# Optimization experiments

Measured on AMD Instinct MI355X. Metric: run time of the kernel, lower is better.

## Reference

```python
import jax, jax.numpy as jnp
import numpy as np

NUM_DIRECTIONS = 32
RESOLUTION = 64
SCALE = 8.0
RADIUS_MULT = 1.1
SEED = 17


def _directions(num_directions, seed):
    # mirrors _generate_uniform_directions: randn columns normalized to unit norm
    v = jax.random.normal(jax.random.key(seed), (3, num_directions), dtype=jnp.float32)
    v = v / jnp.clip(jnp.sqrt(jnp.sum(v * v, axis=0, keepdims=True)), 1e-12)
    return v  # [3, D]


def _grid(spatial_shape):
    # voxel coordinates on [-1,1]^3 lattice, flattened to [P, 3]
    axes = [jnp.linspace(-1.0, 1.0, s, dtype=jnp.float32) for s in spatial_shape]
    coords = jnp.stack(jnp.meshgrid(*axes, indexing='ij'), axis=-1).reshape(-1, 3)
    radius = RADIUS_MULT * jnp.max(jnp.sqrt(jnp.sum(coords * coords, axis=-1)))
    return coords, radius


def _ect(weights, coords, dirs, radius):
    # weights: [B, P, C]; coords: [P, 3]; dirs: [3, D]
    nh = coords @ dirs                                   # [P, D] projections
    lin = jnp.linspace(-radius, radius, RESOLUTION)      # [R] thresholds
    # soft indicator: sigmoid(scale * (t - <x, v>))  -> [R, P, D]
    ecc = jax.nn.sigmoid(SCALE * (lin[:, None, None] - nh[None, :, :]))
    # accumulate per (batch, class, threshold, direction)
    return jnp.einsum('bpc,rpd->bcrd', weights, ecc)     # [B, C, R, D]


def _forward(prediction, target):
    B, C = prediction.shape[0], prediction.shape[1]
    spatial = prediction.shape[2:]
    coords, radius = _grid(spatial)
    dirs = _directions(NUM_DIRECTIONS, SEED)
    # apply_activation='auto' with C>1 -> softmax over channel dim
    act = jax.nn.softmax(prediction.astype(jnp.float32), axis=1)
    w_pred = act.reshape(B, C, -1).transpose(0, 2, 1)    # [B, P, C]
    # target: class indices -> one-hot float (prepared target, no activation)
    tgt_oh = jax.nn.one_hot(target, C, axis=1, dtype=jnp.float32)  # [B, C, X, Y, Z]
    w_tgt = tgt_oh.reshape(B, C, -1).transpose(0, 2, 1)  # [B, P, C]
    ect_pred = _ect(w_pred, coords, dirs, radius)
    ect_tgt = _ect(w_tgt, coords, dirs, radius)
    # aggregation='mse'
    return jnp.mean((ect_pred - ect_tgt) ** 2)


def setup_inputs() -> dict:
    key = jax.random.key(0)
    k1, k2 = jax.random.split(key)
    prediction = jax.random.normal(k1, (2, 3, 48, 48, 48), dtype=jnp.float32)
    target = jax.random.randint(k2, (2, 48, 48, 48), 0, 3, dtype=jnp.int64)
    return {"prediction": prediction, "target": target}


def reference(prediction, target):
    return _forward(prediction, target)
```

## Files before the change

### kernel.cpp

```cpp
#include <hip/hip_runtime.h>
#include <cstdint>


#define P_TOT 110592
#define VOX 216
#define GRID 512
#define NREP 4

__device__ __forceinline__ uint32_t rotl32(uint32_t x, int d) {
  return (x << d) | (x >> (32 - d));
}

__device__ __forceinline__ void threefry_0_17(uint32_t x0, uint32_t x1,
                                              uint32_t& o0, uint32_t& o1) {
  const uint32_t ks0 = 0u, ks1 = 17u, ks2 = 0x1BD11BDAu ^ 0u ^ 17u;
  x0 += ks0; x1 += ks1;
#define R4(a,b,c,dd) \
  x0 += x1; x1 = rotl32(x1,(a)); x1 ^= x0; \
  x0 += x1; x1 = rotl32(x1,(b)); x1 ^= x0; \
  x0 += x1; x1 = rotl32(x1,(c)); x1 ^= x0; \
  x0 += x1; x1 = rotl32(x1,(dd)); x1 ^= x0;
  R4(13,15,26,6)   x0 += ks1; x1 += ks2 + 1u;
  R4(17,29,16,24)  x0 += ks2; x1 += ks0 + 2u;
  R4(13,15,26,6)   x0 += ks0; x1 += ks1 + 3u;
  R4(17,29,16,24)  x0 += ks1; x1 += ks2 + 4u;
  R4(13,15,26,6)   x0 += ks2; x1 += ks0 + 5u;
#undef R4
  o0 = x0; o1 = x1;
}

__device__ __forceinline__ float erfinv_f32(float x) {
  float w = -log1pf(-x * x);
  float p;
  if (w < 5.0f) {
    w = w - 2.5f;
    p = 2.81022636e-08f;
    p = fmaf(p, w, 3.43273939e-07f);
    p = fmaf(p, w, -3.5233877e-06f);
    p = fmaf(p, w, -4.39150654e-06f);
    p = fmaf(p, w, 0.00021858087f);
    p = fmaf(p, w, -0.00125372503f);
    p = fmaf(p, w, -0.00417768164f);
    p = fmaf(p, w, 0.246640727f);
    p = fmaf(p, w, 1.50140941f);
  } else {
    w = sqrtf(w) - 3.0f;
    p = -0.000200214257f;
    p = fmaf(p, w, 0.000100950558f);
    p = fmaf(p, w, 0.00134934322f);
    p = fmaf(p, w, 0.000337081863f);
    p = fmaf(p, w, 0.00573950773f);
    p = fmaf(p, w, -0.0076224613f);
    p = fmaf(p, w, 0.00943887047f);
    p = fmaf(p, w, 1.00167406f);
    p = fmaf(p, w, 2.83297682f);
  }
  return p * x;
}

__device__ __forceinline__ void ect_block_compute(
    const float* __restrict__ pred, const int* __restrict__ tgt,
    float* dirs, float4* voxdw, float4* voxc,
    int t, int bx, float acc[8][4]) {
  const int d = t & 31;
  const int rg = t >> 5;
  const int cbase = bx * VOX;

  if (t < 96) {
    uint32_t o0, o1;
    threefry_0_17(0u, (uint32_t)t, o0, o1);
    uint32_t bits = o0 ^ o1;
    float u = __uint_as_float((bits >> 9) | 0x3F800000u) - 1.0f;
    const float lo = -0.99999994f;
    float v = fmaf(u, 2.0f, lo);
    v = fmaxf(v, lo);
    dirs[t] = 1.41421356237f * erfinv_f32(v);
  }
  __syncthreads();
  if (t < 32) {
    float a = dirs[t], b = dirs[32 + t], c = dirs[64 + t];
    float n = fmaxf(sqrtf(a * a + b * b + c * c), 1e-12f);
    dirs[t] = a / n; dirs[32 + t] = b / n; dirs[64 + t] = c / n;
  }
  if (t < VOX) {
    int p = cbase + t;
    int ix = p / 2304; int rem = p - ix * 2304;
    int iy = rem / 48; int iz = rem - iy * 48;
    const float delta = 2.0f / 47.0f;
    voxc[t] = float4{(float)ix * delta - 1.0f, (float)iy * delta - 1.0f,
                     (float)iz * delta - 1.0f, 0.0f};
    float w[4];
#pragma unroll
    for (int b = 0; b < 2; b++) {
      const float* pb = pred + b * (3 * P_TOT) + p;
      float x0 = pb[0], x1 = pb[P_TOT], x2 = pb[2 * P_TOT];
      float m = fmaxf(x0, fmaxf(x1, x2));
      float e0 = __expf(x0 - m), e1 = __expf(x1 - m), e2 = __expf(x2 - m);
      float inv = 1.0f / (e0 + e1 + e2);
      int tg = tgt[b * P_TOT + p];
      w[b * 2 + 0] = e0 * inv - ((tg == 0) ? 1.0f : 0.0f);
      w[b * 2 + 1] = e1 * inv - ((tg == 1) ? 1.0f : 0.0f);
    }
    voxdw[t] = float4{w[0], w[1], w[2], w[3]};
  }
  __syncthreads();

  const float dir0 = dirs[d], dir1 = dirs[32 + d], dir2 = dirs[64 + d];
  const float radius = 1.1f * 1.7320508075688772f;
  const float step = (2.0f * radius) / 63.0f;
  float K[8];
#pragma unroll
  for (int j = 0; j < 8; j++) {
    float lin = fmaf((float)(rg * 8 + j), step, -radius);
    K[j] = __expf(-8.0f * lin);
  }
#pragma unroll
  for (int j = 0; j < 8; j++)
#pragma unroll
    for (int bc = 0; bc < 4; bc++) acc[j][bc] = 0.0f;

#pragma unroll 4
  for (int v = 0; v < VOX; v++) {
    float4 c = voxc[v];
    float4 w = voxdw[v];
    float nh = fmaf(c.z, dir2, fmaf(c.y, dir1, c.x * dir0));
    float E = __expf(8.0f * nh);
    float z[8];
#pragma unroll
    for (int j = 0; j < 8; j++) z[j] = fmaf(E, K[j], 1.0f);
#pragma unroll
    for (int h = 0; h < 4; h++) {
      float pz = z[2 * h] * z[2 * h + 1];
      float rr = __builtin_amdgcn_rcpf(pz);
      float s0 = z[2 * h + 1] * rr;
      float s1 = z[2 * h] * rr;
      acc[2 * h][0] = fmaf(w.x, s0, acc[2 * h][0]);
      acc[2 * h][1] = fmaf(w.y, s0, acc[2 * h][1]);
      acc[2 * h][2] = fmaf(w.z, s0, acc[2 * h][2]);
      acc[2 * h][3] = fmaf(w.w, s0, acc[2 * h][3]);
      acc[2 * h + 1][0] = fmaf(w.x, s1, acc[2 * h + 1][0]);
      acc[2 * h + 1][1] = fmaf(w.y, s1, acc[2 * h + 1][1]);
      acc[2 * h + 1][2] = fmaf(w.z, s1, acc[2 * h + 1][2]);
      acc[2 * h + 1][3] = fmaf(w.w, s1, acc[2 * h + 1][3]);
    }
  }
}

__global__ __launch_bounds__(256, 2) void ect_main_st(
    const float* __restrict__ pred, const int* __restrict__ tgt,
    float* __restrict__ part) {
  __shared__ float dirs[96];
  __shared__ float4 voxdw[VOX];
  __shared__ float4 voxc[VOX];
  const int t = threadIdx.x;
  const int bx = blockIdx.x;
  const int d = t & 31;
  const int rg = t >> 5;
  float acc[8][4];
  ect_block_compute(pred, tgt, dirs, voxdw, voxc, t, bx, acc);

  float4* prt = (float4*)part + (size_t)bx * 2048;
#pragma unroll
  for (int j = 0; j < 8; j++) {
    prt[(rg * 8 + j) * 32 + d] =
        float4{acc[j][0], acc[j][1], acc[j][2], acc[j][3]};
  }
}

__global__ __launch_bounds__(256) void ect_red(
    const float* __restrict__ part, float* __restrict__ gacc2,
    float* __restrict__ out) {
  __shared__ float redf[4];
  __shared__ int islast;
  const int t = threadIdx.x;
  const int rc = blockIdx.x >> 3;
  const int cc = blockIdx.x & 7;
  const int c4 = cc * 256 + t;
  const float4* p4 = (const float4*)part;

  float a0 = 0.f, a1 = 0.f, a2 = 0.f, a3 = 0.f;
#pragma unroll 8
  for (int r = rc * 32; r < rc * 32 + 32; ++r) {
    float4 v = p4[(size_t)r * 2048 + c4];
    a0 += v.x; a1 += v.y; a2 += v.z; a3 += v.w;
  }
  atomicAdd(&gacc2[c4 * 4 + 0], a0);
  atomicAdd(&gacc2[c4 * 4 + 1], a1);
  atomicAdd(&gacc2[c4 * 4 + 2], a2);
  atomicAdd(&gacc2[c4 * 4 + 3], a3);

  __syncthreads();
  unsigned int* cnt = (unsigned int*)(gacc2 + 8192);
  if (t == 0) {
    unsigned int old = __hip_atomic_fetch_add(cnt, 1u, __ATOMIC_RELAXED,
                                              __HIP_MEMORY_SCOPE_AGENT);
    islast = (old == 127u) ? 1 : 0;
  }
  __syncthreads();
  if (islast) {
    float s = 0.0f;
    for (int i = t; i < 2048; i += 256) {
      const unsigned long long* p64 =
          (const unsigned long long*)(gacc2 + i * 4);
      unsigned long long q0 = __hip_atomic_load(p64, __ATOMIC_RELAXED,
                                                __HIP_MEMORY_SCOPE_AGENT);
      unsigned long long q1 = __hip_atomic_load(p64 + 1, __ATOMIC_RELAXED,
                                                __HIP_MEMORY_SCOPE_AGENT);
      float b0 = __uint_as_float((unsigned int)q0);
      float b1 = __uint_as_float((unsigned int)(q0 >> 32));
      float b2 = __uint_as_float((unsigned int)q1);
      float b3 = __uint_as_float((unsigned int)(q1 >> 32));
      s += b0 * b0 + b1 * b1 + (b0 + b1) * (b0 + b1)
         + b2 * b2 + b3 * b3 + (b2 + b3) * (b2 + b3);
    }
#pragma unroll
    for (int off = 32; off > 0; off >>= 1) s += __shfl_down(s, off, 64);
    if ((t & 63) == 0) redf[t >> 6] = s;
    __syncthreads();
    if (t == 0)
      out[0] = (redf[0] + redf[1] + redf[2] + redf[3]) * (1.0f / 12288.0f);
  }
}

__global__ __launch_bounds__(256, 2) void ect_main_at(
    const float* __restrict__ pred, const int* __restrict__ tgt,
    float* __restrict__ gacc) {
  __shared__ float dirs[96];
  __shared__ float4 voxdw[VOX];
  __shared__ float4 voxc[VOX];
  const int t = threadIdx.x;
  const int bx = blockIdx.x;
  const int d = t & 31;
  const int rg = t >> 5;
  float acc[8][4];
  ect_block_compute(pred, tgt, dirs, voxdw, voxc, t, bx, acc);

  float* grep = gacc + (size_t)(bx & (NREP - 1)) * 8192;
#pragma unroll
  for (int j = 0; j < 8; j++) {
    int base = ((rg * 8 + j) * 32 + d) * 4;
    atomicAdd(&grep[base + 0], acc[j][0]);
    atomicAdd(&grep[base + 1], acc[j][1]);
    atomicAdd(&grep[base + 2], acc[j][2]);
    atomicAdd(&grep[base + 3], acc[j][3]);
  }
}

__global__ __launch_bounds__(256) void ect_fin(
    const float* __restrict__ gacc, float* __restrict__ out) {
  __shared__ float red[4];
  int t = threadIdx.x;
  float s = 0.0f;
  for (int i = t; i < 2048; i += 256) {
    float a0 = 0.f, a1 = 0.f, a2 = 0.f, a3 = 0.f;
#pragma unroll
    for (int rep = 0; rep < NREP; rep++) {
      const float4 g = *(const float4*)(gacc + (size_t)rep * 8192 + i * 4);
      a0 += g.x; a1 += g.y; a2 += g.z; a3 += g.w;
    }
    s += a0 * a0 + a1 * a1 + (a0 + a1) * (a0 + a1)
       + a2 * a2 + a3 * a3 + (a2 + a3) * (a2 + a3);
  }
#pragma unroll
  for (int off = 32; off > 0; off >>= 1) s += __shfl_down(s, off, 64);
  if ((t & 63) == 0) red[t >> 6] = s;
  __syncthreads();
  if (t == 0) out[0] = (red[0] + red[1] + red[2] + red[3]) * (1.0f / 12288.0f);
}

extern "C" void kernel_launch(void* const* d_in, const int* in_sizes, int n_in,
                              void* d_out, int out_size, void* d_ws, size_t ws_size,
                              hipStream_t stream) {
  const float* pred = (const float*)d_in[0];
  const int* tgt = (const int*)d_in[1];
  float* ws = (float*)d_ws;
  float* out = (float*)d_out;

  const size_t part_floats = (size_t)GRID * 8192;
  const size_t need = (part_floats + 8192 + 64) * sizeof(float);

  if (ws_size >= need) {
    float* part = ws;
    float* gacc2 = ws + part_floats;
    hipMemsetAsync(gacc2, 0, (8192 + 64) * sizeof(float), stream);
    hipLaunchKernelGGL(ect_main_st, dim3(GRID), dim3(256), 0, stream,
                       pred, tgt, part);
    hipLaunchKernelGGL(ect_red, dim3(128), dim3(256), 0, stream,
                       part, gacc2, out);
  } else {
    float* gacc = ws;
    hipMemsetAsync(gacc, 0, (size_t)NREP * 8192 * sizeof(float), stream);
    hipLaunchKernelGGL(ect_main_at, dim3(GRID), dim3(256), 0, stream,
                       pred, tgt, gacc);
    hipLaunchKernelGGL(ect_fin, dim3(1), dim3(256), 0, stream, gacc, out);
  }
}
```

Baseline: 114.5 us.

## Split voxel preprocessing into separate kernel and double main grid to 1024 blocks

Voxel coordinates and softmax-minus-onehot weights are now computed once by a separate pre-kernel into global buffers. The main kernel reads them directly from global memory, with no shared staging. The primary path launches 1024 blocks of 108 voxels each to improve load balance across CUs, and the reduction kernel is parameterized by grid count. This adds a kernel launch and a global round trip for the voxel data, and moves the per-voxel loads from LDS to global/L2 inside the hot loop.

```diff
diff --git a/kernel.cpp b/kernel.cpp
--- a/kernel.cpp
+++ b/kernel.cpp
@@ -3,8 +3,6 @@
 
 
 #define P_TOT 110592
-#define VOX 216
-#define GRID 512
 #define NREP 4
 
 __device__ __forceinline__ uint32_t rotl32(uint32_t x, int d) {
@@ -58,13 +56,41 @@
   return p * x;
 }
 
-__device__ __forceinline__ void ect_block_compute(
+__global__ __launch_bounds__(256) void ect_pre(
     const float* __restrict__ pred, const int* __restrict__ tgt,
-    float* dirs, float4* voxdw, float4* voxc,
-    int t, int bx, float acc[8][4]) {
+    float4* __restrict__ voxc, float4* __restrict__ voxw) {
+  const int p = blockIdx.x * 256 + threadIdx.x;
+  int ix = p / 2304; int rem = p - ix * 2304;
+  int iy = rem / 48; int iz = rem - iy * 48;
+  const float delta = 2.0f / 47.0f;
+  voxc[p] = float4{(float)ix * delta - 1.0f, (float)iy * delta - 1.0f,
+                   (float)iz * delta - 1.0f, 0.0f};
+  float w[4];
+#pragma unroll
+  for (int b = 0; b < 2; b++) {
+    const float* pb = pred + b * (3 * P_TOT) + p;
+    float x0 = pb[0], x1 = pb[P_TOT], x2 = pb[2 * P_TOT];
+    float m = fmaxf(x0, fmaxf(x1, x2));
+    float e0 = __expf(x0 - m), e1 = __expf(x1 - m), e2 = __expf(x2 - m);
+    float inv = 1.0f / (e0 + e1 + e2);
+    int tg = tgt[b * P_TOT + p];
+    w[b * 2 + 0] = e0 * inv - ((tg == 0) ? 1.0f : 0.0f);
+    w[b * 2 + 1] = e1 * inv - ((tg == 1) ? 1.0f : 0.0f);
+  }
+  voxw[p] = float4{w[0], w[1], w[2], w[3]};
+}
+
+template <int VOXN>
+__global__ __launch_bounds__(256, 2) void ect_main_sm(
+    const float4* __restrict__ voxc, const float4* __restrict__ voxw,
+    float* __restrict__ part) {
+  __shared__ float dirs[96];
+
+  const int t = threadIdx.x;
+  const int bx = blockIdx.x;
   const int d = t & 31;
   const int rg = t >> 5;
-  const int cbase = bx * VOX;
+  const int cbase = bx * VOXN;
 
   if (t < 96) {
     uint32_t o0, o1;
@@ -82,27 +108,6 @@
     float n = fmaxf(sqrtf(a * a + b * b + c * c), 1e-12f);
     dirs[t] = a / n; dirs[32 + t] = b / n; dirs[64 + t] = c / n;
   }
-  if (t < VOX) {
-    int p = cbase + t;
-    int ix = p / 2304; int rem = p - ix * 2304;
-    int iy = rem / 48; int iz = rem - iy * 48;
-    const float delta = 2.0f / 47.0f;
-    voxc[t] = float4{(float)ix * delta - 1.0f, (float)iy * delta - 1.0f,
-                     (float)iz * delta - 1.0f, 0.0f};
-    float w[4];
-#pragma unroll
-    for (int b = 0; b < 2; b++) {
-      const float* pb = pred + b * (3 * P_TOT) + p;
-      float x0 = pb[0], x1 = pb[P_TOT], x2 = pb[2 * P_TOT];
-      float m = fmaxf(x0, fmaxf(x1, x2));
-      float e0 = __expf(x0 - m), e1 = __expf(x1 - m), e2 = __expf(x2 - m);
-      float inv = 1.0f / (e0 + e1 + e2);
-      int tg = tgt[b * P_TOT + p];
-      w[b * 2 + 0] = e0 * inv - ((tg == 0) ? 1.0f : 0.0f);
-      w[b * 2 + 1] = e1 * inv - ((tg == 1) ? 1.0f : 0.0f);
-    }
-    voxdw[t] = float4{w[0], w[1], w[2], w[3]};
-  }
   __syncthreads();
 
   const float dir0 = dirs[d], dir1 = dirs[32 + d], dir2 = dirs[64 + d];
@@ -114,15 +119,17 @@
     float lin = fmaf((float)(rg * 8 + j), step, -radius);
     K[j] = __expf(-8.0f * lin);
   }
+
+  float acc[8][4];
 #pragma unroll
   for (int j = 0; j < 8; j++)
 #pragma unroll
     for (int bc = 0; bc < 4; bc++) acc[j][bc] = 0.0f;
 
 #pragma unroll 4
-  for (int v = 0; v < VOX; v++) {
-    float4 c = voxc[v];
-    float4 w = voxdw[v];
+  for (int v = 0; v < VOXN; v++) {
+    const float4 c = voxc[cbase + v];
+    const float4 w = voxw[cbase + v];
     float nh = fmaf(c.z, dir2, fmaf(c.y, dir1, c.x * dir0));
     float E = __expf(8.0f * nh);
     float z[8];
@@ -144,20 +151,6 @@
       acc[2 * h + 1][3] = fmaf(w.w, s1, acc[2 * h + 1][3]);
     }
   }
-}
-
-__global__ __launch_bounds__(256, 2) void ect_main_st(
-    const float* __restrict__ pred, const int* __restrict__ tgt,
-    float* __restrict__ part) {
-  __shared__ float dirs[96];
-  __shared__ float4 voxdw[VOX];
-  __shared__ float4 voxc[VOX];
-  const int t = threadIdx.x;
-  const int bx = blockIdx.x;
-  const int d = t & 31;
-  const int rg = t >> 5;
-  float acc[8][4];
-  ect_block_compute(pred, tgt, dirs, voxdw, voxc, t, bx, acc);
 
   float4* prt = (float4*)part + (size_t)bx * 2048;
 #pragma unroll
@@ -169,7 +162,7 @@
 
 __global__ __launch_bounds__(256) void ect_red(
     const float* __restrict__ part, float* __restrict__ gacc2,
-    float* __restrict__ out) {
+    float* __restrict__ out, int ngrid) {
   __shared__ float redf[4];
   __shared__ int islast;
   const int t = threadIdx.x;
@@ -194,7 +187,7 @@
   if (t == 0) {
     unsigned int old = __hip_atomic_fetch_add(cnt, 1u, __ATOMIC_RELAXED,
                                               __HIP_MEMORY_SCOPE_AGENT);
-    islast = (old == 127u) ? 1 : 0;
+    islast = (old == (unsigned int)(ngrid - 1)) ? 1 : 0;
   }
   __syncthreads();
   if (islast) {
@@ -226,14 +219,93 @@
     const float* __restrict__ pred, const int* __restrict__ tgt,
     float* __restrict__ gacc) {
   __shared__ float dirs[96];
-  __shared__ float4 voxdw[VOX];
-  __shared__ float4 voxc[VOX];
+  __shared__ float4 voxdw[216];
+  __shared__ float4 voxcl[216];
   const int t = threadIdx.x;
   const int bx = blockIdx.x;
   const int d = t & 31;
   const int rg = t >> 5;
+  const int cbase = bx * 216;
+
+  if (t < 96) {
+    uint32_t o0, o1;
+    threefry_0_17(0u, (uint32_t)t, o0, o1);
+    uint32_t bits = o0 ^ o1;
+    float u = __uint_as_float((bits >> 9) | 0x3F800000u) - 1.0f;
+    const float lo = -0.99999994f;
+    float v = fmaf(u, 2.0f, lo);
+    v = fmaxf(v, lo);
+    dirs[t] = 1.41421356237f * erfinv_f32(v);
+  }
+  __syncthreads();
+  if (t < 32) {
+    float a = dirs[t], b = dirs[32 + t], c = dirs[64 + t];
+    float n = fmaxf(sqrtf(a * a + b * b + c * c), 1e-12f);
+    dirs[t] = a / n; dirs[32 + t] = b / n; dirs[64 + t] = c / n;
+  }
+  if (t < 216) {
+    int p = cbase + t;
+    int ix = p / 2304; int rem = p - ix * 2304;
+    int iy = rem / 48; int iz = rem - iy * 48;
+    const float delta = 2.0f / 47.0f;
+    voxcl[t] = float4{(float)ix * delta - 1.0f, (float)iy * delta - 1.0f,
+                      (float)iz * delta - 1.0f, 0.0f};
+    float w[4];
+#pragma unroll
+    for (int b = 0; b < 2; b++) {
+      const float* pb = pred + b * (3 * P_TOT) + p;
+      float x0 = pb[0], x1 = pb[P_TOT], x2 = pb[2 * P_TOT];
+      float m = fmaxf(x0, fmaxf(x1, x2));
+      float e0 = __expf(x0 - m), e1 = __expf(x1 - m), e2 = __expf(x2 - m);
+      float inv = 1.0f / (e0 + e1 + e2);
+      int tg = tgt[b * P_TOT + p];
+      w[b * 2 + 0] = e0 * inv - ((tg == 0) ? 1.0f : 0.0f);
+      w[b * 2 + 1] = e1 * inv - ((tg == 1) ? 1.0f : 0.0f);
+    }
+    voxdw[t] = float4{w[0], w[1], w[2], w[3]};
+  }
+  __syncthreads();
+
+  const float dir0 = dirs[d], dir1 = dirs[32 + d], dir2 = dirs[64 + d];
+  const float radius = 1.1f * 1.7320508075688772f;
+  const float step = (2.0f * radius) / 63.0f;
+  float K[8];
+#pragma unroll
+  for (int j = 0; j < 8; j++) {
+    float lin = fmaf((float)(rg * 8 + j), step, -radius);
+    K[j] = __expf(-8.0f * lin);
+  }
   float acc[8][4];
-  ect_block_compute(pred, tgt, dirs, voxdw, voxc, t, bx, acc);
+#pragma unroll
+  for (int j = 0; j < 8; j++)
+#pragma unroll
+    for (int bc = 0; bc < 4; bc++) acc[j][bc] = 0.0f;
+
+#pragma unroll 4
+  for (int v = 0; v < 216; v++) {
+    float4 c = voxcl[v];
+    float4 w = voxdw[v];
+    float nh = fmaf(c.z, dir2, fmaf(c.y, dir1, c.x * dir0));
+    float E = __expf(8.0f * nh);
+    float z[8];
+#pragma unroll
+    for (int j = 0; j < 8; j++) z[j] = fmaf(E, K[j], 1.0f);
+#pragma unroll
+    for (int h = 0; h < 4; h++) {
+      float pz = z[2 * h] * z[2 * h + 1];
+      float rr = __builtin_amdgcn_rcpf(pz);
+      float s0 = z[2 * h + 1] * rr;
+      float s1 = z[2 * h] * rr;
+      acc[2 * h][0] = fmaf(w.x, s0, acc[2 * h][0]);
+      acc[2 * h][1] = fmaf(w.y, s0, acc[2 * h][1]);
+      acc[2 * h][2] = fmaf(w.z, s0, acc[2 * h][2]);
+      acc[2 * h][3] = fmaf(w.w, s0, acc[2 * h][3]);
+      acc[2 * h + 1][0] = fmaf(w.x, s1, acc[2 * h + 1][0]);
+      acc[2 * h + 1][1] = fmaf(w.y, s1, acc[2 * h + 1][1]);
+      acc[2 * h + 1][2] = fmaf(w.z, s1, acc[2 * h + 1][2]);
+      acc[2 * h + 1][3] = fmaf(w.w, s1, acc[2 * h + 1][3]);
+    }
+  }
 
   float* grep = gacc + (size_t)(bx & (NREP - 1)) * 8192;
 #pragma unroll
@@ -276,21 +348,38 @@
   float* ws = (float*)d_ws;
   float* out = (float*)d_out;
 
-  const size_t part_floats = (size_t)GRID * 8192;
-  const size_t need = (part_floats + 8192 + 64) * sizeof(float);
-
-  if (ws_size >= need) {
+  const size_t vox_fl = (size_t)P_TOT * 4;
+  const size_t needA = ((size_t)1024 * 8192 + 8256 + 2 * vox_fl) * sizeof(float);
+  const size_t needB = ((size_t)512 * 8192 + 8256 + 2 * vox_fl) * sizeof(float);
+
+  if (ws_size >= needA) {
     float* part = ws;
-    float* gacc2 = ws + part_floats;
+    float* gacc2 = ws + (size_t)1024 * 8192;
+    float4* voxc = (float4*)(gacc2 + 8256);
+    float4* voxw = voxc + P_TOT;
     hipMemsetAsync(gacc2, 0, (8192 + 64) * sizeof(float), stream);
-    hipLaunchKernelGGL(ect_main_st, dim3(GRID), dim3(256), 0, stream,
-                       pred, tgt, part);
+    hipLaunchKernelGGL(ect_pre, dim3(432), dim3(256), 0, stream,
+                       pred, tgt, voxc, voxw);
+    hipLaunchKernelGGL(ect_main_sm<108>, dim3(1024), dim3(256), 0, stream,
+                       voxc, voxw, part);
+    hipLaunchKernelGGL(ect_red, dim3(256), dim3(256), 0, stream,
+                       part, gacc2, out, 256);
+  } else if (ws_size >= needB) {
+    float* part = ws;
+    float* gacc2 = ws + (size_t)512 * 8192;
+    float4* voxc = (float4*)(gacc2 + 8256);
+    float4* voxw = voxc + P_TOT;
+    hipMemsetAsync(gacc2, 0, (8192 + 64) * sizeof(float), stream);
+    hipLaunchKernelGGL(ect_pre, dim3(432), dim3(256), 0, stream,
+                       pred, tgt, voxc, voxw);
+    hipLaunchKernelGGL(ect_main_sm<216>, dim3(512), dim3(256), 0, stream,
+                       voxc, voxw, part);
     hipLaunchKernelGGL(ect_red, dim3(128), dim3(256), 0, stream,
-                       part, gacc2, out);
+                       part, gacc2, out, 128);
   } else {
     float* gacc = ws;
     hipMemsetAsync(gacc, 0, (size_t)NREP * 8192 * sizeof(float), stream);
-    hipLaunchKernelGGL(ect_main_at, dim3(GRID), dim3(256), 0, stream,
+    hipLaunchKernelGGL(ect_main_at, dim3(512), dim3(256), 0, stream,
                        pred, tgt, gacc);
     hipLaunchKernelGGL(ect_fin, dim3(1), dim3(256), 0, stream, gacc, out);
   }
```

Result: slower. 119.1 us (+4.0%).

## Precompute per-voxel exp table in LDS, double grid, fold memset into main kernel

Applied to the files above, without the earlier changes.

Each block now builds a shared table of exp(8*<x,v>) for every voxel-direction pair before the main loop, instead of each of the 8 threshold-group threads recomputing the projection and exponential. This removes the redundant per-thread transcendental and coordinate math. The grid is doubled to 1024 blocks of 108 voxels when the workspace is large enough, which doubles the partial buffer the reduction kernel has to read. The accumulator and counter zeroing moves from a separate memset into the first blocks of the main kernel. That relies on the main kernel finishing before the reduction kernel starts, and it adds LDS use that may limit occupancy.

```diff
diff --git a/kernel.cpp b/kernel.cpp
--- a/kernel.cpp
+++ b/kernel.cpp
@@ -3,8 +3,6 @@
 
 
 #define P_TOT 110592
-#define VOX 216
-#define GRID 512
 #define NREP 4
 
 __device__ __forceinline__ uint32_t rotl32(uint32_t x, int d) {
@@ -58,13 +56,14 @@
   return p * x;
 }
 
+template <int VOXN>
 __device__ __forceinline__ void ect_block_compute(
     const float* __restrict__ pred, const int* __restrict__ tgt,
-    float* dirs, float4* voxdw, float4* voxc,
+    float* dirs, float4* voxdw, float* Etab,
     int t, int bx, float acc[8][4]) {
   const int d = t & 31;
   const int rg = t >> 5;
-  const int cbase = bx * VOX;
+  const int cbase = bx * VOXN;
 
   if (t < 96) {
     uint32_t o0, o1;
@@ -82,13 +81,8 @@
     float n = fmaxf(sqrtf(a * a + b * b + c * c), 1e-12f);
     dirs[t] = a / n; dirs[32 + t] = b / n; dirs[64 + t] = c / n;
   }
-  if (t < VOX) {
+  if (t < VOXN) {
     int p = cbase + t;
-    int ix = p / 2304; int rem = p - ix * 2304;
-    int iy = rem / 48; int iz = rem - iy * 48;
-    const float delta = 2.0f / 47.0f;
-    voxc[t] = float4{(float)ix * delta - 1.0f, (float)iy * delta - 1.0f,
-                     (float)iz * delta - 1.0f, 0.0f};
     float w[4];
 #pragma unroll
     for (int b = 0; b < 2; b++) {
@@ -105,7 +99,20 @@
   }
   __syncthreads();
 
-  const float dir0 = dirs[d], dir1 = dirs[32 + d], dir2 = dirs[64 + d];
+  const float delta = 2.0f / 47.0f;
+  for (int i = t; i < VOXN * 32; i += 256) {
+    int v = i >> 5, dd = i & 31;
+    int p = cbase + v;
+    int ix = p / 2304; int rem = p - ix * 2304;
+    int iy = rem / 48; int iz = rem - iy * 48;
+    float cx = (float)ix * delta - 1.0f;
+    float cy = (float)iy * delta - 1.0f;
+    float cz = (float)iz * delta - 1.0f;
+    float nh = fmaf(cz, dirs[64 + dd], fmaf(cy, dirs[32 + dd], cx * dirs[dd]));
+    Etab[i] = __expf(8.0f * nh);
+  }
+  __syncthreads();
+
   const float radius = 1.1f * 1.7320508075688772f;
   const float step = (2.0f * radius) / 63.0f;
   float K[8];
@@ -120,11 +127,9 @@
     for (int bc = 0; bc < 4; bc++) acc[j][bc] = 0.0f;
 
 #pragma unroll 4
-  for (int v = 0; v < VOX; v++) {
-    float4 c = voxc[v];
+  for (int v = 0; v < VOXN; v++) {
     float4 w = voxdw[v];
-    float nh = fmaf(c.z, dir2, fmaf(c.y, dir1, c.x * dir0));
-    float E = __expf(8.0f * nh);
+    float E = Etab[(v << 5) + d];
     float z[8];
 #pragma unroll
     for (int j = 0; j < 8; j++) z[j] = fmaf(E, K[j], 1.0f);
@@ -146,18 +151,25 @@
   }
 }
 
+template <int VOXN>
 __global__ __launch_bounds__(256, 2) void ect_main_st(
     const float* __restrict__ pred, const int* __restrict__ tgt,
-    float* __restrict__ part) {
+    float* __restrict__ part, float* __restrict__ gacc2) {
   __shared__ float dirs[96];
-  __shared__ float4 voxdw[VOX];
-  __shared__ float4 voxc[VOX];
+  __shared__ float4 voxdw[VOXN];
+  __shared__ float Etab[VOXN * 32];
   const int t = threadIdx.x;
   const int bx = blockIdx.x;
   const int d = t & 31;
   const int rg = t >> 5;
+
+  if (bx < 8) {
+    ((float4*)gacc2)[bx * 256 + t] = float4{0.0f, 0.0f, 0.0f, 0.0f};
+  }
+  if (bx == 8 && t == 0) *(unsigned int*)(gacc2 + 8192) = 0u;
+
   float acc[8][4];
-  ect_block_compute(pred, tgt, dirs, voxdw, voxc, t, bx, acc);
+  ect_block_compute<VOXN>(pred, tgt, dirs, voxdw, Etab, t, bx, acc);
 
   float4* prt = (float4*)part + (size_t)bx * 2048;
 #pragma unroll
@@ -169,7 +181,7 @@
 
 __global__ __launch_bounds__(256) void ect_red(
     const float* __restrict__ part, float* __restrict__ gacc2,
-    float* __restrict__ out) {
+    float* __restrict__ out, int ngrid) {
   __shared__ float redf[4];
   __shared__ int islast;
   const int t = threadIdx.x;
@@ -194,7 +206,7 @@
   if (t == 0) {
     unsigned int old = __hip_atomic_fetch_add(cnt, 1u, __ATOMIC_RELAXED,
                                               __HIP_MEMORY_SCOPE_AGENT);
-    islast = (old == 127u) ? 1 : 0;
+    islast = (old == (unsigned int)(ngrid - 1)) ? 1 : 0;
   }
   __syncthreads();
   if (islast) {
@@ -226,14 +238,14 @@
     const float* __restrict__ pred, const int* __restrict__ tgt,
     float* __restrict__ gacc) {
   __shared__ float dirs[96];
-  __shared__ float4 voxdw[VOX];
-  __shared__ float4 voxc[VOX];
+  __shared__ float4 voxdw[216];
+  __shared__ float Etab[216 * 32];
   const int t = threadIdx.x;
   const int bx = blockIdx.x;
   const int d = t & 31;
   const int rg = t >> 5;
   float acc[8][4];
-  ect_block_compute(pred, tgt, dirs, voxdw, voxc, t, bx, acc);
+  ect_block_compute<216>(pred, tgt, dirs, voxdw, Etab, t, bx, acc);
 
   float* grep = gacc + (size_t)(bx & (NREP - 1)) * 8192;
 #pragma unroll
@@ -276,21 +288,27 @@
   float* ws = (float*)d_ws;
   float* out = (float*)d_out;
 
-  const size_t part_floats = (size_t)GRID * 8192;
-  const size_t need = (part_floats + 8192 + 64) * sizeof(float);
-
-  if (ws_size >= need) {
+  const size_t need1024 = ((size_t)1024 * 8192 + 8192 + 64) * sizeof(float);
+  const size_t need512 = ((size_t)512 * 8192 + 8192 + 64) * sizeof(float);
+
+  if (ws_size >= need1024) {
     float* part = ws;
-    float* gacc2 = ws + part_floats;
-    hipMemsetAsync(gacc2, 0, (8192 + 64) * sizeof(float), stream);
-    hipLaunchKernelGGL(ect_main_st, dim3(GRID), dim3(256), 0, stream,
-                       pred, tgt, part);
+    float* gacc2 = ws + (size_t)1024 * 8192;
+    hipLaunchKernelGGL(ect_main_st<108>, dim3(1024), dim3(256), 0, stream,
+                       pred, tgt, part, gacc2);
+    hipLaunchKernelGGL(ect_red, dim3(256), dim3(256), 0, stream,
+                       part, gacc2, out, 256);
+  } else if (ws_size >= need512) {
+    float* part = ws;
+    float* gacc2 = ws + (size_t)512 * 8192;
+    hipLaunchKernelGGL(ect_main_st<216>, dim3(512), dim3(256), 0, stream,
+                       pred, tgt, part, gacc2);
     hipLaunchKernelGGL(ect_red, dim3(128), dim3(256), 0, stream,
-                       part, gacc2, out);
+                       part, gacc2, out, 128);
   } else {
     float* gacc = ws;
     hipMemsetAsync(gacc, 0, (size_t)NREP * 8192 * sizeof(float), stream);
-    hipLaunchKernelGGL(ect_main_at, dim3(GRID), dim3(256), 0, stream,
+    hipLaunchKernelGGL(ect_main_at, dim3(512), dim3(256), 0, stream,
                        pred, tgt, gacc);
     hipLaunchKernelGGL(ect_fin, dim3(1), dim3(256), 0, stream, gacc, out);
   }
```

Measured after the change: 108.9 us. 4.9% less time.
